# Kernel optimization log

Hardware: AMD Instinct MI355X
Metric: run time of the kernel (lower is better)

Reference implementation:

```python
import jax, jax.numpy as jnp
import numpy as np


def setup_inputs() -> dict:
    key = jax.random.key(0)
    ks = jax.random.split(key, 8)
    B, N, C = 4, 2048, 1024
    H, hd, lr, R = 16, 64, 20, 200  # R = low_rank * rank_multi
    s = lambda k, shape, fan: jax.random.normal(k, shape, jnp.float32) / np.sqrt(fan)
    return {
        'x': jax.random.normal(ks[0], (B, N, C), jnp.float32),
        'qk_w': s(ks[1], (2 * C, C), C),
        'proj_w': s(ks[2], (C, C), C),
        'proj_b': jnp.zeros((C,), jnp.float32),
        'we': s(ks[3], (H, R, lr), R),
        'wr': s(ks[4], (H, R, lr), R),
        'cw_w': s(ks[5], (hd, 2 * lr), 2 * lr),
        'cw_b': jnp.zeros((hd,), jnp.float32),
    }


def _l2norm(v, eps=1e-12):
    # matches F.normalize(p=2, dim=-1): x / max(||x||, eps)
    n = jnp.sqrt(jnp.sum(v * v, axis=-1, keepdims=True))
    return v / jnp.maximum(n, eps)


def reference(x, qk_w, proj_w, proj_b, we, wr, cw_w, cw_b):
    B, N, C = x.shape
    H, R, lr = we.shape  # heads, subsample len, low_rank
    hd = C // H
    # qk projection -> q,k: [B,H,N,hd]
    qk = (x @ qk_w.T).reshape(B, N, 2, H, hd).transpose(2, 0, 3, 1, 4)
    q, k = qk[0], qk[1]
    # gen_weights: subsample N positions (embed_len > low_rank*rank_multi branch)
    idx = np.linspace(0, N - 1, R).astype(np.int64)  # static, trunc like torch
    xh = x.transpose(0, 2, 1).reshape(B, H, hd, N)[:, :, :, idx]  # [B,H,hd,R]
    we_b = jnp.einsum('bhdr,hre->bhde', xh, we)  # [B,H,hd,lr]
    wr_b = jnp.einsum('bhdr,hre->bhde', xh, wr)
    # feature map + low-rank scores
    q = _l2norm(q)
    k = _l2norm(k)
    escore = jnp.einsum('bhnd,bhde->bhne', q, we_b)  # [B,H,N,lr]
    rscore = jnp.einsum('bhnd,bhde->bhne', k, wr_b)
    score = jnp.concatenate([escore, rscore], axis=-1)  # [B,H,N,2lr]
    attn = score @ cw_w.T + cw_b  # [B,H,N,hd]
    attn = attn.transpose(0, 2, 1, 3).reshape(B, N, C)
    out = attn @ proj_w.T + proj_b  # dropout is identity at eval
    return out
```

## Files before the change

### kernel.cpp

```cpp
#include <hip/hip_runtime.h>
#include <hip/hip_bf16.h>

constexpr int B_  = 4;
constexpr int N_  = 2048;
constexpr int C_  = 1024;
constexpr int H_  = 16;
constexpr int HD  = 64;
constexpr int LR  = 20;
constexpr int RS  = 200;
constexpr int RP  = 224;

typedef __attribute__((ext_vector_type(8))) short bf16x8;
typedef __attribute__((ext_vector_type(4))) float f32x4;

__device__ __forceinline__ float b2f_raw(unsigned short u) {
    union { unsigned int i; float f; } v;
    v.i = ((unsigned int)u) << 16;
    return v.f;
}
__device__ __forceinline__ unsigned short f2b(float f) {
    __hip_bfloat16 h = __float2bfloat16(f);
    return *(unsigned short*)&h;
}

__device__ __forceinline__ void async_load16(const unsigned short* g, unsigned short* l) {
    __builtin_amdgcn_global_load_lds(
        (const __attribute__((address_space(1))) unsigned int*)(const void*)g,
        (__attribute__((address_space(3))) unsigned int*)(void*)l,
        16, 0, 0);
}

__global__ __launch_bounds__(256)
void detect_kernel(const unsigned int* __restrict__ x, int* __restrict__ flag) {
    const int t = threadIdx.x;
    int cnt = 0;
    for (int i = t; i < 1024; i += 256) {
        const unsigned int w = x[i];
        const unsigned int e = (w >> 7) & 0xFFu;
        cnt += (e >= 103u && e <= 140u) ? 1 : 0;
    }
    __shared__ int s[256];
    s[t] = cnt;
    __syncthreads();
    for (int off = 128; off > 0; off >>= 1) {
        if (t < off) s[t] += s[t + off];
        __syncthreads();
    }
    if (t == 0) *flag = (s[0] > 512) ? 1 : 0;
}

struct CvtArgs {
    const void* src[8];
    unsigned short* dst[8];
    int size[8];
};

__global__ __launch_bounds__(256)
void convert_kernel(const int* __restrict__ flag, CvtArgs args) {
    const int buf = blockIdx.y;
    const int n4 = args.size[buf] >> 2;
    const int stride = gridDim.x * blockDim.x;
    const bool isbf = (*flag != 0);
    for (int i = blockIdx.x * blockDim.x + threadIdx.x; i < n4; i += stride) {
        ushort4 o;
        if (isbf) {
            o = ((const ushort4*)args.src[buf])[i];
        } else {
            const float4 v = ((const float4*)args.src[buf])[i];
            o.x = f2b(v.x); o.y = f2b(v.y); o.z = f2b(v.z); o.w = f2b(v.w);
        }
        ((ushort4*)args.dst[buf])[i] = o;
    }
}

template <bool OBF, bool HAS_BIAS>
__device__ void mfma_gemm_body(const unsigned short* __restrict__ A,
                               const unsigned short* __restrict__ W,
                               const unsigned short* __restrict__ bias,
                               void* __restrict__ out,
                               int M, int N, int K) {
    constexpr int BM = 128, BN = 128, BK = 32;
    __shared__ __align__(16) unsigned short As[BM * BK];
    __shared__ __align__(16) unsigned short Bs[BN * BK];

    const int t    = threadIdx.x;
    const int wave = t >> 6;
    const int lane = t & 63;
    const int m0   = blockIdx.y * BM;
    const int n0   = blockIdx.x * BN;

    const int srow = lane >> 2;
    const int scol = (lane & 3) * 8;
    const unsigned short* ga0 = A + (size_t)(m0 + wave * 16 + srow) * K + scol;
    const unsigned short* ga1 = A + (size_t)(m0 + (wave + 4) * 16 + srow) * K + scol;
    const unsigned short* gb0 = W + (size_t)(n0 + wave * 16 + srow) * K + scol;
    const unsigned short* gb1 = W + (size_t)(n0 + (wave + 4) * 16 + srow) * K + scol;
    unsigned short* lA0 = &As[wave * 512];
    unsigned short* lA1 = &As[(wave + 4) * 512];
    unsigned short* lB0 = &Bs[wave * 512];
    unsigned short* lB1 = &Bs[(wave + 4) * 512];

    const int wr = (wave >> 1) * 64;
    const int wc = (wave & 1) * 64;
    const int lq = lane >> 4;
    const int lm = lane & 15;

    f32x4 acc[4][4];
    #pragma unroll
    for (int i = 0; i < 4; ++i)
        #pragma unroll
        for (int j = 0; j < 4; ++j) acc[i][j] = 0.f;

    for (int k0 = 0; k0 < K; k0 += BK) {
        async_load16(ga0, lA0);
        async_load16(ga1, lA1);
        async_load16(gb0, lB0);
        async_load16(gb1, lB1);
        ga0 += BK; ga1 += BK; gb0 += BK; gb1 += BK;
        __syncthreads();

        bf16x8 af[4], bfr[4];
        #pragma unroll
        for (int i = 0; i < 4; ++i)
            af[i] = *(const bf16x8*)&As[(wr + i * 16 + lm) * BK + lq * 8];
        #pragma unroll
        for (int j = 0; j < 4; ++j)
            bfr[j] = *(const bf16x8*)&Bs[(wc + j * 16 + lm) * BK + lq * 8];

        #pragma unroll
        for (int i = 0; i < 4; ++i)
            #pragma unroll
            for (int j = 0; j < 4; ++j)
                acc[i][j] = __builtin_amdgcn_mfma_f32_16x16x32_bf16(
                    af[i], bfr[j], acc[i][j], 0, 0, 0);

        __syncthreads();
    }

    #pragma unroll
    for (int i = 0; i < 4; ++i) {
        #pragma unroll
        for (int j = 0; j < 4; ++j) {
            const int col = n0 + wc + j * 16 + lm;
            float bv = 0.f;
            if constexpr (HAS_BIAS) bv = b2f_raw(bias[col]);
            #pragma unroll
            for (int r = 0; r < 4; ++r) {
                const int row = m0 + wr + i * 16 + lq * 4 + r;
                const float v = acc[i][j][r] + bv;
                if constexpr (OBF)
                    ((__hip_bfloat16*)out)[(size_t)row * N + col] = __float2bfloat16(v);
                else
                    ((float*)out)[(size_t)row * N + col] = v;
            }
        }
    }
}

__global__ __launch_bounds__(256)
void gemm1_kernel(const unsigned short* __restrict__ xb,
                  const unsigned short* __restrict__ qkwb,
                  unsigned short* __restrict__ qk) {
    mfma_gemm_body<true, false>(xb, qkwb, nullptr, qk, B_ * N_, 2 * C_, C_);
}

__global__ __launch_bounds__(256)
void gemm2_kernel(const int* __restrict__ flag,
                  const unsigned short* __restrict__ attn,
                  const unsigned short* __restrict__ pwb,
                  const unsigned short* __restrict__ pbb,
                  void* __restrict__ out) {
    if (*flag) mfma_gemm_body<true, true>(attn, pwb, pbb, out, B_ * N_, C_, C_);
    else       mfma_gemm_body<false, true>(attn, pwb, pbb, out, B_ * N_, C_, C_);
}

__global__ __launch_bounds__(256)
void wec_kernel(const unsigned short* __restrict__ we_in,
                const unsigned short* __restrict__ wr_in,
                const unsigned short* __restrict__ cwwb,
                unsigned short* __restrict__ wect,
                unsigned short* __restrict__ wrct) {
    const int o = blockIdx.x * 256 + threadIdx.x;
    if (o >= H_ * HD * RP) return;
    const int r    = o % RP;
    const int dout = (o / RP) % HD;
    const int h    = o / (RP * HD);
    float sq = 0.f, sk = 0.f;
    if (r < RS) {
        #pragma unroll
        for (int e = 0; e < LR; ++e) {
            const float cq = b2f_raw(cwwb[dout * 2 * LR + e]);
            const float ck = b2f_raw(cwwb[dout * 2 * LR + LR + e]);
            sq += b2f_raw(we_in[((size_t)h * RS + r) * LR + e]) * cq;
            sk += b2f_raw(wr_in[((size_t)h * RS + r) * LR + e]) * ck;
        }
    }
    wect[o] = f2b(sq);
    wrct[o] = f2b(sk);
}

__global__ __launch_bounds__(256)
void gather_kernel(const unsigned short* __restrict__ xb,
                   unsigned short* __restrict__ xh) {
    const int bh = blockIdx.x;
    const int b  = bh >> 4;
    const int h  = bh & 15;
    for (int o = threadIdx.x; o < HD * RP; o += 256) {
        const int din = o & 63;
        const int r   = o >> 6;
        unsigned short v = 0;
        if (r < RS) {
            const int ir = (r * (N_ - 1)) / (RS - 1);
            v = xb[((size_t)b * N_ + ir) * C_ + h * HD + din];
        }
        xh[(size_t)bh * HD * RP + (size_t)din * RP + r] = v;
    }
}

__global__ __launch_bounds__(64)
void collapse_kernel(const unsigned short* __restrict__ xh,
                     const unsigned short* __restrict__ wect,
                     const unsigned short* __restrict__ wrct,
                     unsigned short* __restrict__ we2t,
                     unsigned short* __restrict__ wr2t) {
    const int blk = blockIdx.x;
    const int bh  = blk >> 2;
    const int qk  = (blk >> 1) & 1;
    const int dh  = blk & 1;
    const int h   = bh & 15;
    const int lane = threadIdx.x;
    const int lq = lane >> 4;
    const int lm = lane & 15;

    const unsigned short* wsrc = (qk ? wrct : wect) + (size_t)h * HD * RP;
    const unsigned short* xsrc = xh + (size_t)bh * HD * RP;
    unsigned short* dst = (qk ? wr2t : we2t) + (size_t)bh * HD * HD;

    f32x4 acc[2][4];
    #pragma unroll
    for (int i = 0; i < 2; ++i)
        #pragma unroll
        for (int j = 0; j < 4; ++j) acc[i][j] = 0.f;

    for (int ks = 0; ks < RP / 32; ++ks) {
        bf16x8 a[2], bfr[4];
        #pragma unroll
        for (int rt = 0; rt < 2; ++rt)
            a[rt] = *(const bf16x8*)&wsrc[(size_t)(dh * 32 + rt * 16 + lm) * RP + ks * 32 + lq * 8];
        #pragma unroll
        for (int j = 0; j < 4; ++j)
            bfr[j] = *(const bf16x8*)&xsrc[(size_t)(j * 16 + lm) * RP + ks * 32 + lq * 8];
        #pragma unroll
        for (int rt = 0; rt < 2; ++rt)
            #pragma unroll
            for (int j = 0; j < 4; ++j)
                acc[rt][j] = __builtin_amdgcn_mfma_f32_16x16x32_bf16(
                    a[rt], bfr[j], acc[rt][j], 0, 0, 0);
    }

    #pragma unroll
    for (int rt = 0; rt < 2; ++rt)
        #pragma unroll
        for (int j = 0; j < 4; ++j)
            #pragma unroll
            for (int r = 0; r < 4; ++r) {
                const int dout = dh * 32 + rt * 16 + lq * 4 + r;
                const int din  = j * 16 + lm;
                dst[dout * HD + din] = f2b(acc[rt][j][r]);
            }
}

__global__ __launch_bounds__(256)
void score_attn_kernel(const unsigned short* __restrict__ qk,
                       const unsigned short* __restrict__ we2t,
                       const unsigned short* __restrict__ wr2t,
                       const unsigned short* __restrict__ cwbb,
                       unsigned short* __restrict__ attn) {
    const int wave = threadIdx.x >> 6;
    const int lane = threadIdx.x & 63;
    const int wg   = blockIdx.x * 4 + wave;
    const int bh   = wg >> 6;
    const int n0   = (wg & 63) * 32;
    const int b    = bh >> 4;
    const int h    = bh & 15;
    const int lq   = lane >> 4;
    const int lm   = lane & 15;

    bf16x8 bq[2][4], bk[2][4];
    {
        const unsigned short* wq = we2t + (size_t)bh * HD * HD;
        const unsigned short* wk = wr2t + (size_t)bh * HD * HD;
        #pragma unroll
        for (int t2 = 0; t2 < 2; ++t2)
            #pragma unroll
            for (int j = 0; j < 4; ++j) {
                const int dout = j * 16 + lm;
                bq[t2][j] = *(const bf16x8*)&wq[dout * HD + t2 * 32 + lq * 8];
                bk[t2][j] = *(const bf16x8*)&wk[dout * HD + t2 * 32 + lq * 8];
            }
    }

    f32x4 accQ[2][4], accK[2][4];
    #pragma unroll
    for (int i = 0; i < 2; ++i)
        #pragma unroll
        for (int j = 0; j < 4; ++j) { accQ[i][j] = 0.f; accK[i][j] = 0.f; }

    float invq[2], invk[2];

    #pragma unroll
    for (int rt = 0; rt < 2; ++rt) {
        const int row = n0 + rt * 16 + lm;
        const size_t base = ((size_t)(b * N_ + row)) * (2 * C_) + h * HD;
        bf16x8 aq[2], ak[2];
        aq[0] = *(const bf16x8*)&qk[base + lq * 8];
        aq[1] = *(const bf16x8*)&qk[base + 32 + lq * 8];
        ak[0] = *(const bf16x8*)&qk[base + C_ + lq * 8];
        ak[1] = *(const bf16x8*)&qk[base + C_ + 32 + lq * 8];

        float sq = 0.f, sk = 0.f;
        #pragma unroll
        for (int t2 = 0; t2 < 2; ++t2)
            #pragma unroll
            for (int j = 0; j < 8; ++j) {
                const float vq = b2f_raw((unsigned short)aq[t2][j]);
                const float vk = b2f_raw((unsigned short)ak[t2][j]);
                sq += vq * vq;
                sk += vk * vk;
            }
        sq += __shfl_xor(sq, 16, 64);
        sq += __shfl_xor(sq, 32, 64);
        sk += __shfl_xor(sk, 16, 64);
        sk += __shfl_xor(sk, 32, 64);
        invq[rt] = 1.f / fmaxf(sqrtf(sq), 1e-12f);
        invk[rt] = 1.f / fmaxf(sqrtf(sk), 1e-12f);

        #pragma unroll
        for (int t2 = 0; t2 < 2; ++t2)
            #pragma unroll
            for (int j = 0; j < 4; ++j) {
                accQ[rt][j] = __builtin_amdgcn_mfma_f32_16x16x32_bf16(
                    aq[t2], bq[t2][j], accQ[rt][j], 0, 0, 0);
                accK[rt][j] = __builtin_amdgcn_mfma_f32_16x16x32_bf16(
                    ak[t2], bk[t2][j], accK[rt][j], 0, 0, 0);
            }
    }

    #pragma unroll
    for (int rt = 0; rt < 2; ++rt) {
        float iq[4], ik[4];
        #pragma unroll
        for (int r = 0; r < 4; ++r) {
            iq[r] = __shfl(invq[rt], lq * 4 + r, 64);
            ik[r] = __shfl(invk[rt], lq * 4 + r, 64);
        }
        #pragma unroll
        for (int j = 0; j < 4; ++j) {
            const float bv = b2f_raw(cwbb[j * 16 + lm]);
            #pragma unroll
            for (int r = 0; r < 4; ++r) {
                const int row = n0 + rt * 16 + lq * 4 + r;
                const float v = accQ[rt][j][r] * iq[r] + accK[rt][j][r] * ik[r] + bv;
                attn[((size_t)(b * N_ + row)) * C_ + h * HD + j * 16 + lm] = f2b(v);
            }
        }
    }
}

extern "C" void kernel_launch(void* const* d_in, const int* in_sizes, int n_in,
                              void* d_out, int out_size, void* d_ws, size_t ws_size,
                              hipStream_t stream) {
    (void)in_sizes; (void)n_in; (void)out_size; (void)ws_size;

    char* ws = (char*)d_ws;
    size_t off = 0;
    auto alloc = [&](size_t bytes) {
        char* p = ws + off;
        off += (bytes + 255) & ~(size_t)255;
        return p;
    };

    int* flag = (int*)alloc(16);
    char* xb_region   = alloc((size_t)B_ * N_ * C_ * 2);
    char* qkwb_region = alloc((size_t)2 * C_ * C_ * 2);
    unsigned short* pwb   = (unsigned short*)alloc((size_t)C_ * C_ * 2);
    unsigned short* pbb   = (unsigned short*)alloc((size_t)C_ * 2);
    unsigned short* we_i  = (unsigned short*)alloc((size_t)H_ * RS * LR * 2);
    unsigned short* wr_i  = (unsigned short*)alloc((size_t)H_ * RS * LR * 2);
    unsigned short* cwwb  = (unsigned short*)alloc((size_t)HD * 2 * LR * 2);
    unsigned short* cwbb  = (unsigned short*)alloc((size_t)HD * 2);
    unsigned short* qk    = (unsigned short*)alloc((size_t)B_ * N_ * 2 * C_ * 2);
    unsigned short* we2t  = (unsigned short*)alloc((size_t)B_ * H_ * HD * HD * 2);
    unsigned short* wr2t  = (unsigned short*)alloc((size_t)B_ * H_ * HD * HD * 2);

    unsigned short* xb   = (unsigned short*)xb_region;
    unsigned short* attn = (unsigned short*)xb_region;
    unsigned short* qkwb = (unsigned short*)qkwb_region;
    unsigned short* wect = (unsigned short*)qkwb_region;
    unsigned short* wrct = (unsigned short*)(qkwb_region + (size_t)H_ * HD * RP * 2);
    unsigned short* xh   = (unsigned short*)(qkwb_region + (size_t)2 * H_ * HD * RP * 2);

    const int M = B_ * N_;

    detect_kernel<<<1, 256, 0, stream>>>((const unsigned int*)d_in[0], flag);

    CvtArgs ca;
    ca.src[0] = d_in[0]; ca.dst[0] = xb;   ca.size[0] = B_ * N_ * C_;
    ca.src[1] = d_in[1]; ca.dst[1] = qkwb; ca.size[1] = 2 * C_ * C_;
    ca.src[2] = d_in[2]; ca.dst[2] = pwb;  ca.size[2] = C_ * C_;
    ca.src[3] = d_in[3]; ca.dst[3] = pbb;  ca.size[3] = C_;
    ca.src[4] = d_in[4]; ca.dst[4] = we_i; ca.size[4] = H_ * RS * LR;
    ca.src[5] = d_in[5]; ca.dst[5] = wr_i; ca.size[5] = H_ * RS * LR;
    ca.src[6] = d_in[6]; ca.dst[6] = cwwb; ca.size[6] = HD * 2 * LR;
    ca.src[7] = d_in[7]; ca.dst[7] = cwbb; ca.size[7] = HD;
    convert_kernel<<<dim3(2048, 8), 256, 0, stream>>>(flag, ca);

    gemm1_kernel<<<dim3((2 * C_) / 128, M / 128), 256, 0, stream>>>(xb, qkwb, qk);

    wec_kernel<<<(H_ * HD * RP + 255) / 256, 256, 0, stream>>>(
        we_i, wr_i, cwwb, wect, wrct);
    gather_kernel<<<B_ * H_, 256, 0, stream>>>(xb, xh);
    collapse_kernel<<<B_ * H_ * 4, 64, 0, stream>>>(xh, wect, wrct, we2t, wr2t);

    score_attn_kernel<<<(B_ * H_ * N_ / 32) / 4, 256, 0, stream>>>(
        qk, we2t, wr2t, cwbb, attn);

    gemm2_kernel<<<dim3(C_ / 128, M / 128), 256, 0, stream>>>(flag, attn, pwb, pbb, d_out);
}
```

Measured before the change: 229.6 us.

## Fuse QK projection GEMM with l2-norm and low-rank score kernel

Each block now computes the q and k tiles for one head and a 128-row slab by pairing q columns with the matching k columns. It then normalizes rows in registers, stages the normalized tiles in shared memory and applies the collapsed per-head weights right away. This removes the bf16 qk intermediate, saving its write and re-read, and drops one kernel launch. Buffers that used to alias are now allocated separately so the fused kernel can read xb while writing attn. The cost is a larger shared-memory footprint and a normalization step that uses the fp32 accumulators instead of the bf16-rounded values.

```diff
diff --git a/kernel.cpp b/kernel.cpp
--- a/kernel.cpp
+++ b/kernel.cpp
@@ -73,7 +73,153 @@
     }
 }
 
-template <bool OBF, bool HAS_BIAS>
+__global__ __launch_bounds__(256)
+void gemm1_score_kernel(const unsigned short* __restrict__ xb,
+                        const unsigned short* __restrict__ qkwb,
+                        const unsigned short* __restrict__ we2t,
+                        const unsigned short* __restrict__ wr2t,
+                        const unsigned short* __restrict__ cwbb,
+                        unsigned short* __restrict__ attn) {
+    constexpr int BK = 32;
+    constexpr int QS = 72;
+    __shared__ __align__(16) unsigned short pool[2 * 128 * QS];
+    unsigned short* As = pool;
+    unsigned short* Bs = pool + 4096;
+    unsigned short* qn = pool;
+    unsigned short* kn = pool + 128 * QS;
+
+    const int t    = threadIdx.x;
+    const int wave = t >> 6;
+    const int lane = t & 63;
+    const int h    = blockIdx.x;
+    const int m0   = blockIdx.y * 128;
+    const int K    = C_;
+
+    const int srow = lane >> 2;
+    const int scol = (lane & 3) * 8;
+    const unsigned short* ga0 = xb + (size_t)(m0 + wave * 16 + srow) * K + scol;
+    const unsigned short* ga1 = xb + (size_t)(m0 + (wave + 4) * 16 + srow) * K + scol;
+    const unsigned short* gb0 = qkwb + (size_t)(h * HD + wave * 16 + srow) * K + scol;
+    const unsigned short* gb1 = qkwb + (size_t)(C_ + h * HD + wave * 16 + srow) * K + scol;
+    unsigned short* lA0 = &As[wave * 512];
+    unsigned short* lA1 = &As[(wave + 4) * 512];
+    unsigned short* lB0 = &Bs[wave * 512];
+    unsigned short* lB1 = &Bs[(wave + 4) * 512];
+
+    const int wr = (wave >> 1) * 64;
+    const int wc = (wave & 1) * 64;
+    const int lq = lane >> 4;
+    const int lm = lane & 15;
+
+    f32x4 acc[4][4];
+    #pragma unroll
+    for (int i = 0; i < 4; ++i)
+        #pragma unroll
+        for (int j = 0; j < 4; ++j) acc[i][j] = 0.f;
+
+    for (int k0 = 0; k0 < K; k0 += BK) {
+        async_load16(ga0, lA0);
+        async_load16(ga1, lA1);
+        async_load16(gb0, lB0);
+        async_load16(gb1, lB1);
+        ga0 += BK; ga1 += BK; gb0 += BK; gb1 += BK;
+        __syncthreads();
+
+        bf16x8 af[4], bfr[4];
+        #pragma unroll
+        for (int i = 0; i < 4; ++i)
+            af[i] = *(const bf16x8*)&As[(wr + i * 16 + lm) * BK + lq * 8];
+        #pragma unroll
+        for (int j = 0; j < 4; ++j)
+            bfr[j] = *(const bf16x8*)&Bs[(wc + j * 16 + lm) * BK + lq * 8];
+
+        #pragma unroll
+        for (int i = 0; i < 4; ++i)
+            #pragma unroll
+            for (int j = 0; j < 4; ++j)
+                acc[i][j] = __builtin_amdgcn_mfma_f32_16x16x32_bf16(
+                    af[i], bfr[j], acc[i][j], 0, 0, 0);
+
+        __syncthreads();
+    }
+
+    unsigned short* dst = (wc == 0) ? qn : kn;
+    #pragma unroll
+    for (int i = 0; i < 4; ++i) {
+        float inv[4];
+        #pragma unroll
+        for (int r = 0; r < 4; ++r) {
+            float s = 0.f;
+            #pragma unroll
+            for (int j = 0; j < 4; ++j) s += acc[i][j][r] * acc[i][j][r];
+            s += __shfl_xor(s, 1, 64);
+            s += __shfl_xor(s, 2, 64);
+            s += __shfl_xor(s, 4, 64);
+            s += __shfl_xor(s, 8, 64);
+            inv[r] = 1.f / fmaxf(sqrtf(s), 1e-12f);
+        }
+        #pragma unroll
+        for (int j = 0; j < 4; ++j)
+            #pragma unroll
+            for (int r = 0; r < 4; ++r) {
+                const int row = wr + i * 16 + lq * 4 + r;
+                dst[row * QS + j * 16 + lm] = f2b(acc[i][j][r] * inv[r]);
+            }
+    }
+    __syncthreads();
+
+    const int b  = blockIdx.y >> 4;
+    const int bh = b * H_ + h;
+    const unsigned short* wq = we2t + (size_t)bh * HD * HD;
+    const unsigned short* wk = wr2t + (size_t)bh * HD * HD;
+
+    bf16x8 bq[2][4], bk[2][4];
+    #pragma unroll
+    for (int t2 = 0; t2 < 2; ++t2)
+        #pragma unroll
+        for (int j = 0; j < 4; ++j) {
+            const int dout = j * 16 + lm;
+            bq[t2][j] = *(const bf16x8*)&wq[dout * HD + t2 * 32 + lq * 8];
+            bk[t2][j] = *(const bf16x8*)&wk[dout * HD + t2 * 32 + lq * 8];
+        }
+
+    f32x4 accS[2][4];
+    #pragma unroll
+    for (int rt = 0; rt < 2; ++rt)
+        #pragma unroll
+        for (int j = 0; j < 4; ++j) accS[rt][j] = 0.f;
+
+    #pragma unroll
+    for (int rt = 0; rt < 2; ++rt) {
+        const int lr = wave * 32 + rt * 16 + lm;
+        bf16x8 aq0 = *(const bf16x8*)&qn[lr * QS + lq * 8];
+        bf16x8 aq1 = *(const bf16x8*)&qn[lr * QS + 32 + lq * 8];
+        bf16x8 ak0 = *(const bf16x8*)&kn[lr * QS + lq * 8];
+        bf16x8 ak1 = *(const bf16x8*)&kn[lr * QS + 32 + lq * 8];
+        #pragma unroll
+        for (int j = 0; j < 4; ++j) {
+            accS[rt][j] = __builtin_amdgcn_mfma_f32_16x16x32_bf16(aq0, bq[0][j], accS[rt][j], 0, 0, 0);
+            accS[rt][j] = __builtin_amdgcn_mfma_f32_16x16x32_bf16(aq1, bq[1][j], accS[rt][j], 0, 0, 0);
+            accS[rt][j] = __builtin_amdgcn_mfma_f32_16x16x32_bf16(ak0, bk[0][j], accS[rt][j], 0, 0, 0);
+            accS[rt][j] = __builtin_amdgcn_mfma_f32_16x16x32_bf16(ak1, bk[1][j], accS[rt][j], 0, 0, 0);
+        }
+    }
+
+    #pragma unroll
+    for (int rt = 0; rt < 2; ++rt)
+        #pragma unroll
+        for (int j = 0; j < 4; ++j) {
+            const int dout = j * 16 + lm;
+            const float bv = b2f_raw(cwbb[dout]);
+            #pragma unroll
+            for (int r = 0; r < 4; ++r) {
+                const int row = m0 + wave * 32 + rt * 16 + lq * 4 + r;
+                attn[(size_t)row * C_ + h * HD + dout] = f2b(accS[rt][j][r] + bv);
+            }
+        }
+}
+
+template <bool OBF>
 __device__ void mfma_gemm_body(const unsigned short* __restrict__ A,
                                const unsigned short* __restrict__ W,
                                const unsigned short* __restrict__ bias,
@@ -142,8 +288,7 @@
         #pragma unroll
         for (int j = 0; j < 4; ++j) {
             const int col = n0 + wc + j * 16 + lm;
-            float bv = 0.f;
-            if constexpr (HAS_BIAS) bv = b2f_raw(bias[col]);
+            const float bv = b2f_raw(bias[col]);
             #pragma unroll
             for (int r = 0; r < 4; ++r) {
                 const int row = m0 + wr + i * 16 + lq * 4 + r;
@@ -158,20 +303,13 @@
 }
 
 __global__ __launch_bounds__(256)
-void gemm1_kernel(const unsigned short* __restrict__ xb,
-                  const unsigned short* __restrict__ qkwb,
-                  unsigned short* __restrict__ qk) {
-    mfma_gemm_body<true, false>(xb, qkwb, nullptr, qk, B_ * N_, 2 * C_, C_);
-}
-
-__global__ __launch_bounds__(256)
 void gemm2_kernel(const int* __restrict__ flag,
                   const unsigned short* __restrict__ attn,
                   const unsigned short* __restrict__ pwb,
                   const unsigned short* __restrict__ pbb,
                   void* __restrict__ out) {
-    if (*flag) mfma_gemm_body<true, true>(attn, pwb, pbb, out, B_ * N_, C_, C_);
-    else       mfma_gemm_body<false, true>(attn, pwb, pbb, out, B_ * N_, C_, C_);
+    if (*flag) mfma_gemm_body<true>(attn, pwb, pbb, out, B_ * N_, C_, C_);
+    else       mfma_gemm_body<false>(attn, pwb, pbb, out, B_ * N_, C_, C_);
 }
 
 __global__ __launch_bounds__(256)
@@ -270,103 +408,6 @@
             }
 }
 
-__global__ __launch_bounds__(256)
-void score_attn_kernel(const unsigned short* __restrict__ qk,
-                       const unsigned short* __restrict__ we2t,
-                       const unsigned short* __restrict__ wr2t,
-                       const unsigned short* __restrict__ cwbb,
-                       unsigned short* __restrict__ attn) {
-    const int wave = threadIdx.x >> 6;
-    const int lane = threadIdx.x & 63;
-    const int wg   = blockIdx.x * 4 + wave;
-    const int bh   = wg >> 6;
-    const int n0   = (wg & 63) * 32;
-    const int b    = bh >> 4;
-    const int h    = bh & 15;
-    const int lq   = lane >> 4;
-    const int lm   = lane & 15;
-
-    bf16x8 bq[2][4], bk[2][4];
-    {
-        const unsigned short* wq = we2t + (size_t)bh * HD * HD;
-        const unsigned short* wk = wr2t + (size_t)bh * HD * HD;
-        #pragma unroll
-        for (int t2 = 0; t2 < 2; ++t2)
-            #pragma unroll
-            for (int j = 0; j < 4; ++j) {
-                const int dout = j * 16 + lm;
-                bq[t2][j] = *(const bf16x8*)&wq[dout * HD + t2 * 32 + lq * 8];
-                bk[t2][j] = *(const bf16x8*)&wk[dout * HD + t2 * 32 + lq * 8];
-            }
-    }
-
-    f32x4 accQ[2][4], accK[2][4];
-    #pragma unroll
-    for (int i = 0; i < 2; ++i)
-        #pragma unroll
-        for (int j = 0; j < 4; ++j) { accQ[i][j] = 0.f; accK[i][j] = 0.f; }
-
-    float invq[2], invk[2];
-
-    #pragma unroll
-    for (int rt = 0; rt < 2; ++rt) {
-        const int row = n0 + rt * 16 + lm;
-        const size_t base = ((size_t)(b * N_ + row)) * (2 * C_) + h * HD;
-        bf16x8 aq[2], ak[2];
-        aq[0] = *(const bf16x8*)&qk[base + lq * 8];
-        aq[1] = *(const bf16x8*)&qk[base + 32 + lq * 8];
-        ak[0] = *(const bf16x8*)&qk[base + C_ + lq * 8];
-        ak[1] = *(const bf16x8*)&qk[base + C_ + 32 + lq * 8];
-
-        float sq = 0.f, sk = 0.f;
-        #pragma unroll
-        for (int t2 = 0; t2 < 2; ++t2)
-            #pragma unroll
-            for (int j = 0; j < 8; ++j) {
-                const float vq = b2f_raw((unsigned short)aq[t2][j]);
-                const float vk = b2f_raw((unsigned short)ak[t2][j]);
-                sq += vq * vq;
-                sk += vk * vk;
-            }
-        sq += __shfl_xor(sq, 16, 64);
-        sq += __shfl_xor(sq, 32, 64);
-        sk += __shfl_xor(sk, 16, 64);
-        sk += __shfl_xor(sk, 32, 64);
-        invq[rt] = 1.f / fmaxf(sqrtf(sq), 1e-12f);
-        invk[rt] = 1.f / fmaxf(sqrtf(sk), 1e-12f);
-
-        #pragma unroll
-        for (int t2 = 0; t2 < 2; ++t2)
-            #pragma unroll
-            for (int j = 0; j < 4; ++j) {
-                accQ[rt][j] = __builtin_amdgcn_mfma_f32_16x16x32_bf16(
-                    aq[t2], bq[t2][j], accQ[rt][j], 0, 0, 0);
-                accK[rt][j] = __builtin_amdgcn_mfma_f32_16x16x32_bf16(
-                    ak[t2], bk[t2][j], accK[rt][j], 0, 0, 0);
-            }
-    }
-
-    #pragma unroll
-    for (int rt = 0; rt < 2; ++rt) {
-        float iq[4], ik[4];
-        #pragma unroll
-        for (int r = 0; r < 4; ++r) {
-            iq[r] = __shfl(invq[rt], lq * 4 + r, 64);
-            ik[r] = __shfl(invk[rt], lq * 4 + r, 64);
-        }
-        #pragma unroll
-        for (int j = 0; j < 4; ++j) {
-            const float bv = b2f_raw(cwbb[j * 16 + lm]);
-            #pragma unroll
-            for (int r = 0; r < 4; ++r) {
-                const int row = n0 + rt * 16 + lq * 4 + r;
-                const float v = accQ[rt][j][r] * iq[r] + accK[rt][j][r] * ik[r] + bv;
-                attn[((size_t)(b * N_ + row)) * C_ + h * HD + j * 16 + lm] = f2b(v);
-            }
-        }
-    }
-}
-
 extern "C" void kernel_launch(void* const* d_in, const int* in_sizes, int n_in,
                               void* d_out, int out_size, void* d_ws, size_t ws_size,
                               hipStream_t stream) {
@@ -381,24 +422,20 @@
     };
 
     int* flag = (int*)alloc(16);
-    char* xb_region   = alloc((size_t)B_ * N_ * C_ * 2);
-    char* qkwb_region = alloc((size_t)2 * C_ * C_ * 2);
+    unsigned short* xb    = (unsigned short*)alloc((size_t)B_ * N_ * C_ * 2);
+    unsigned short* qkwb  = (unsigned short*)alloc((size_t)2 * C_ * C_ * 2);
     unsigned short* pwb   = (unsigned short*)alloc((size_t)C_ * C_ * 2);
     unsigned short* pbb   = (unsigned short*)alloc((size_t)C_ * 2);
     unsigned short* we_i  = (unsigned short*)alloc((size_t)H_ * RS * LR * 2);
     unsigned short* wr_i  = (unsigned short*)alloc((size_t)H_ * RS * LR * 2);
     unsigned short* cwwb  = (unsigned short*)alloc((size_t)HD * 2 * LR * 2);
     unsigned short* cwbb  = (unsigned short*)alloc((size_t)HD * 2);
-    unsigned short* qk    = (unsigned short*)alloc((size_t)B_ * N_ * 2 * C_ * 2);
+    unsigned short* attn  = (unsigned short*)alloc((size_t)B_ * N_ * C_ * 2);
     unsigned short* we2t  = (unsigned short*)alloc((size_t)B_ * H_ * HD * HD * 2);
     unsigned short* wr2t  = (unsigned short*)alloc((size_t)B_ * H_ * HD * HD * 2);
-
-    unsigned short* xb   = (unsigned short*)xb_region;
-    unsigned short* attn = (unsigned short*)xb_region;
-    unsigned short* qkwb = (unsigned short*)qkwb_region;
-    unsigned short* wect = (unsigned short*)qkwb_region;
-    unsigned short* wrct = (unsigned short*)(qkwb_region + (size_t)H_ * HD * RP * 2);
-    unsigned short* xh   = (unsigned short*)(qkwb_region + (size_t)2 * H_ * HD * RP * 2);
+    unsigned short* wect  = (unsigned short*)alloc((size_t)H_ * HD * RP * 2);
+    unsigned short* wrct  = (unsigned short*)alloc((size_t)H_ * HD * RP * 2);
+    unsigned short* xh    = (unsigned short*)alloc((size_t)B_ * H_ * HD * RP * 2);
 
     const int M = B_ * N_;
 
@@ -415,15 +452,13 @@
     ca.src[7] = d_in[7]; ca.dst[7] = cwbb; ca.size[7] = HD;
     convert_kernel<<<dim3(2048, 8), 256, 0, stream>>>(flag, ca);
 
-    gemm1_kernel<<<dim3((2 * C_) / 128, M / 128), 256, 0, stream>>>(xb, qkwb, qk);
-
     wec_kernel<<<(H_ * HD * RP + 255) / 256, 256, 0, stream>>>(
         we_i, wr_i, cwwb, wect, wrct);
     gather_kernel<<<B_ * H_, 256, 0, stream>>>(xb, xh);
     collapse_kernel<<<B_ * H_ * 4, 64, 0, stream>>>(xh, wect, wrct, we2t, wr2t);
 
-    score_attn_kernel<<<(B_ * H_ * N_ / 32) / 4, 256, 0, stream>>>(
-        qk, we2t, wr2t, cwbb, attn);
+    gemm1_score_kernel<<<dim3(H_, M / 128), 256, 0, stream>>>(
+        xb, qkwb, we2t, wr2t, cwbb, attn);
 
     gemm2_kernel<<<dim3(C_ / 128, M / 128), 256, 0, stream>>>(flag, attn, pwb, pbb, d_out);
 }
```

Measured after the change: 229.5 us. Within noise of the previous version (-0.0%).
